# Kernel tuning notes

Hardware: AMD Instinct MI355X
Metric: run time of the kernel (lower is better)

## Reference

```python
import jax, jax.numpy as jnp
import numpy as np

B, C, H, W = 128, 512, 14, 14
P = 512  # num_parts (codebook size)


def setup_inputs() -> dict:
    key = jax.random.key(0)
    k1, k2, k3 = jax.random.split(key, 3)
    fm = jax.random.normal(k1, (B, C, H, W), dtype=jnp.float32)
    embedding = jax.random.normal(k2, (B, C), dtype=jnp.float32)
    # self.w = torch.randn(P, C).clamp_(min=0)
    w = jnp.maximum(jax.random.normal(k3, (P, C), dtype=jnp.float32), 0.0)
    w_ep_sum = w  # clone of w at init
    w_ep_num = jnp.ones((P,), dtype=jnp.float32)
    return {"fm": fm, "embedding": embedding, "w": w,
            "w_ep_sum": w_ep_sum, "w_ep_num": w_ep_num, "epoch": 5}


def reference(fm, embedding, w, w_ep_sum, w_ep_num, epoch):
    b, c, h, wd = fm.shape
    p = w.shape[0]
    # NCHW -> [B, HW, C]
    x = jnp.transpose(fm, (0, 2, 3, 1)).reshape(b, h * wd, c)
    xf = x.reshape(b * h * wd, c)
    dist = (jnp.sum(xf * xf, axis=1, keepdims=True)
            + jnp.sum(w * w, axis=1)
            - 2.0 * (xf @ w.T))                      # [B*HW, P]
    assign = jax.nn.softmax(-dist.reshape(b, h * wd, p), axis=-1)
    # hard threshold: zero out weak assignments
    assign = jnp.where(assign < 1.0 / p, 0.0, assign)  # [B, HW, P]
    assign_sum = assign.mean(axis=1)                    # [B, P]

    if epoch > 2:  # epoch is a static Python int
        # relu(einsum('bn,nc->bnc').mean(1)) == relu((assign_sum @ w) / P)
        cvec = jax.nn.relu((assign_sum @ w) / p)        # [B, C]
        embedding_cat = jnp.concatenate([embedding, cvec], axis=-1)
    else:
        embedding_cat = jnp.concatenate([embedding, jnp.zeros_like(embedding)], axis=-1)

    # collect_weight (no-grad EMA-style accumulate).
    # einsum('bmn,bmc->bmnc').sum(1).sum(0) == einsum('bmn,bmc->nc') -- avoids
    # materializing the [B,M,N,C] tensor the torch code builds.
    update_w = jnp.einsum('bmn,bmc->nc', assign, x)     # [P, C]
    assign_mean = jnp.sum(assign, axis=(0, 1))          # [P]
    upd = assign_mean > 1.0
    new_w_ep_sum = jnp.where(upd[:, None], w_ep_sum + update_w, w_ep_sum)
    new_w_ep_num = jnp.where(upd, w_ep_num + assign_mean, w_ep_num)
    return embedding_cat, new_w_ep_sum, new_w_ep_num
```

## Files before the change

### kernel.cpp

```cpp
#include <hip/hip_runtime.h>
#include <hip/hip_bf16.h>

#define Bn   128
#define Cn   512
#define HWn  196
#define Mn   25088
#define Pn   512
#define MPAD 32768
#define SPLITK2 32
#define KCH  1024

#define OFF_XT     0u
#define OFF_AT     8388608u
#define OFF_PART   16777216u
#define OFF_XMT    16777216u
#define OFF_WF     25165824u
#define OFF_WNORM  25296896u
#define OFF_RAWP   25297408u
#define OFF_MEAN   25559552u

#define OUT_CAT  0u
#define OUT_WSUM 131072u
#define OUT_WNUM 393216u

using bf16x8 = __attribute__((ext_vector_type(8))) short;
using f16x8  = __attribute__((ext_vector_type(8))) _Float16;
using f32x4  = __attribute__((ext_vector_type(4))) float;

__device__ __forceinline__ unsigned short f2b(float f) {
    union { float f; unsigned u; } x; x.f = f;
    unsigned r = x.u + 0x7fffu + ((x.u >> 16) & 1u);
    return (unsigned short)(r >> 16);
}

__global__ __launch_bounds__(64) void k_wnorm(const float* __restrict__ w,
                                              float* __restrict__ wn,
                                              _Float16* __restrict__ wf) {
    int n = blockIdx.x, l = threadIdx.x;
    const float* p = w + (size_t)n * Cn + l * 8;
    float4 a = *(const float4*)p;
    float4 b = *(const float4*)(p + 4);
    float s = a.x*a.x + a.y*a.y + a.z*a.z + a.w*a.w
            + b.x*b.x + b.y*b.y + b.z*b.z + b.w*b.w;
    alignas(16) _Float16 h[8];
    h[0]=(_Float16)a.x; h[1]=(_Float16)a.y; h[2]=(_Float16)a.z; h[3]=(_Float16)a.w;
    h[4]=(_Float16)b.x; h[5]=(_Float16)b.y; h[6]=(_Float16)b.z; h[7]=(_Float16)b.w;
    *(float4*)(wf + (size_t)(n >> 4) * 8192u + (size_t)(l >> 2) * 512
                 + (n & 15) * 32 + (l & 3) * 8) = *(const float4*)h;
    #pragma unroll
    for (int o = 32; o > 0; o >>= 1) s += __shfl_down(s, o);
    if (l == 0) wn[n] = s;
}

__global__ __launch_bounds__(512) void k_prep2(const float* __restrict__ fm,
                                               _Float16* __restrict__ xmt,
                                               unsigned short* __restrict__ xt) {
    __shared__ _Float16 tile[64][200];
    int b = blockIdx.x;
    int cg = blockIdx.y * 64;
    int t = threadIdx.x;
    for (int i = t; i < 64 * 49; i += 512) {
        int cl = i / 49, h4 = i - cl * 49;
        float4 v = *(const float4*)(fm + ((size_t)(b * Cn + cg + cl) * HWn) + h4 * 4);
        tile[cl][h4*4+0] = (_Float16)v.x;
        tile[cl][h4*4+1] = (_Float16)v.y;
        tile[cl][h4*4+2] = (_Float16)v.z;
        tile[cl][h4*4+3] = (_Float16)v.w;
    }
    __syncthreads();
    for (int i = t; i < 2048; i += 512) {
        int q = i >> 9, rem = i & 511, j = rem >> 3, cgi = rem & 7;
        alignas(16) _Float16 h[8];
        if (j < 49) {
            #pragma unroll
            for (int x = 0; x < 8; ++x) h[x] = tile[cgi * 8 + x][q * 49 + j];
        } else {
            #pragma unroll
            for (int x = 0; x < 8; ++x) h[x] = (_Float16)0.f;
        }
        int Ti = b * 16 + q * 4 + (j >> 4);
        int seg = (cg >> 5) + (cgi >> 2);
        int inner = (j & 15) * 32 + (cgi & 3) * 8;
        *(float4*)(xmt + (size_t)Ti * 8192u + (size_t)seg * 512 + inner) = *(const float4*)h;
    }
    for (int i = t; i < 64 * 4 * 16; i += 512) {
        int cl = i >> 6, rem = i & 63;
        int q = rem >> 4, j4 = rem & 15;
        ushort4 o;
        if (j4 < 12) {
            o.x = f2b((float)tile[cl][q*49 + j4*4 + 0]);
            o.y = f2b((float)tile[cl][q*49 + j4*4 + 1]);
            o.z = f2b((float)tile[cl][q*49 + j4*4 + 2]);
            o.w = f2b((float)tile[cl][q*49 + j4*4 + 3]);
        } else if (j4 == 12) {
            o.x = f2b((float)tile[cl][q*49 + 48]);
            o.y = 0; o.z = 0; o.w = 0;
        } else {
            o.x = 0; o.y = 0; o.z = 0; o.w = 0;
        }
        int c = cg + cl;
        int T = c >> 4;
        int seg = b * 8 + q * 2 + (j4 >> 3);
        int k = (j4 & 7) * 4;
        *(ushort4*)(xt + (size_t)T * 524288u + (size_t)seg * 512 + (c & 15) * 32 + k) = o;
    }
}

__global__ __launch_bounds__(512) void k_post(const _Float16* __restrict__ xmt,
                                              const _Float16* __restrict__ wf,
                                              const float* __restrict__ wnorm,
                                              unsigned short* __restrict__ at,
                                              float* __restrict__ rawp) {
    __shared__ float redmx[64][8];
    __shared__ float redsm[64][8];
    const int bid = blockIdx.x;
    const int b = bid >> 2, chunk = bid & 3;
    const int tid = threadIdx.x;
    const int nq = tid >> 6, lane = tid & 63;
    const int rl = lane & 15, rq = lane >> 4;
    const int loff = rl * 32 + rq * 8;
    const int n0 = nq * 64;

    const _Float16* pa[4];
    const _Float16* pb[4];
    #pragma unroll
    for (int f = 0; f < 4; ++f) {
        pa[f] = xmt + (size_t)(b * 16 + chunk * 4 + f) * 8192u + loff;
        pb[f] = wf  + (size_t)(nq * 4 + f) * 8192u + loff;
    }

    f32x4 acc[4][4] = {};
    f16x8 aC[4], bC[4], aN[4], bN[4];
    #pragma unroll
    for (int f = 0; f < 4; ++f) {
        aC[f] = *(const f16x8*)(pa[f]);
        bC[f] = *(const f16x8*)(pb[f]);
    }
    for (int seg = 0; seg < 16; seg += 2) {
        #pragma unroll
        for (int f = 0; f < 4; ++f) {
            aN[f] = *(const f16x8*)(pa[f] + (seg + 1) * 512);
            bN[f] = *(const f16x8*)(pb[f] + (seg + 1) * 512);
        }
        #pragma unroll
        for (int i = 0; i < 4; ++i)
            #pragma unroll
            for (int j = 0; j < 4; ++j)
                acc[i][j] = __builtin_amdgcn_mfma_f32_16x16x32_f16(aC[i], bC[j], acc[i][j], 0, 0, 0);
        if (seg + 2 < 16) {
            #pragma unroll
            for (int f = 0; f < 4; ++f) {
                aC[f] = *(const f16x8*)(pa[f] + (seg + 2) * 512);
                bC[f] = *(const f16x8*)(pb[f] + (seg + 2) * 512);
            }
        }
        #pragma unroll
        for (int i = 0; i < 4; ++i)
            #pragma unroll
            for (int j = 0; j < 4; ++j)
                acc[i][j] = __builtin_amdgcn_mfma_f32_16x16x32_f16(aN[i], bN[j], acc[i][j], 0, 0, 0);
    }
    float wn[4];
    #pragma unroll
    for (int g = 0; g < 4; ++g) wn[g] = wnorm[n0 + g * 16 + rl];
    #pragma unroll
    for (int f = 0; f < 4; ++f)
        #pragma unroll
        for (int g = 0; g < 4; ++g)
            #pragma unroll
            for (int r = 0; r < 4; ++r)
                acc[f][g][r] = 2.0f * acc[f][g][r] - wn[g];
    float mx[4][4];
    #pragma unroll
    for (int f = 0; f < 4; ++f)
        #pragma unroll
        for (int r = 0; r < 4; ++r) {
            float m_ = fmaxf(fmaxf(acc[f][0][r], acc[f][1][r]),
                             fmaxf(acc[f][2][r], acc[f][3][r]));
            #pragma unroll
            for (int o = 8; o >= 1; o >>= 1) m_ = fmaxf(m_, __shfl_xor(m_, o));
            mx[f][r] = m_;
        }
    if (rl == 0)
        #pragma unroll
        for (int f = 0; f < 4; ++f)
            #pragma unroll
            for (int r = 0; r < 4; ++r)
                redmx[f * 16 + rq * 4 + r][nq] = mx[f][r];
    __syncthreads();
    float rmax[4][4];
    #pragma unroll
    for (int f = 0; f < 4; ++f)
        #pragma unroll
        for (int r = 0; r < 4; ++r) {
            const float* q = redmx[f * 16 + rq * 4 + r];
            rmax[f][r] = fmaxf(fmaxf(fmaxf(q[0], q[1]), fmaxf(q[2], q[3])),
                               fmaxf(fmaxf(q[4], q[5]), fmaxf(q[6], q[7])));
        }
    float sm[4][4];
    #pragma unroll
    for (int f = 0; f < 4; ++f)
        #pragma unroll
        for (int r = 0; r < 4; ++r) {
            float s_ = 0.f;
            #pragma unroll
            for (int g = 0; g < 4; ++g) {
                float p = __expf(acc[f][g][r] - rmax[f][r]);
                acc[f][g][r] = p;
                s_ += p;
            }
            #pragma unroll
            for (int o = 8; o >= 1; o >>= 1) s_ += __shfl_xor(s_, o);
            sm[f][r] = s_;
        }
    if (rl == 0)
        #pragma unroll
        for (int f = 0; f < 4; ++f)
            #pragma unroll
            for (int r = 0; r < 4; ++r)
                redsm[f * 16 + rq * 4 + r][nq] = sm[f][r];
    __syncthreads();
    const float invP = 1.0f / 512.0f;
    #pragma unroll
    for (int f = 0; f < 4; ++f)
        #pragma unroll
        for (int r = 0; r < 4; ++r) {
            const float* q = redsm[f * 16 + rq * 4 + r];
            float inv = 1.0f / (q[0] + q[1] + q[2] + q[3] + q[4] + q[5] + q[6] + q[7]);
            #pragma unroll
            for (int g = 0; g < 4; ++g) {
                float a = acc[f][g][r] * inv;
                acc[f][g][r] = (a < invP) ? 0.0f : a;
            }
        }
    float cs[4] = {};
    #pragma unroll
    for (int g = 0; g < 4; ++g) {
        #pragma unroll
        for (int f = 0; f < 4; ++f)
            #pragma unroll
            for (int r = 0; r < 4; ++r)
                if (f * 16 + rq * 4 + r < 49) cs[g] += acc[f][g][r];
        cs[g] += __shfl_xor(cs[g], 16);
        cs[g] += __shfl_xor(cs[g], 32);
    }
    if (rq == 0)
        #pragma unroll
        for (int g = 0; g < 4; ++g)
            rawp[(size_t)bid * 512 + n0 + g * 16 + rl] = cs[g];
    const int segb = b * 8 + chunk * 2;
    #pragma unroll
    for (int f = 0; f < 4; ++f) {
        const int mloc = f * 16 + rq * 4;
        const int sa = segb + (mloc >> 5);
        const int k = mloc & 31;
        #pragma unroll
        for (int g = 0; g < 4; ++g) {
            ushort4 o;
            o.x = (mloc + 0 < 49) ? f2b(acc[f][g][0]) : (unsigned short)0;
            o.y = (mloc + 1 < 49) ? f2b(acc[f][g][1]) : (unsigned short)0;
            o.z = (mloc + 2 < 49) ? f2b(acc[f][g][2]) : (unsigned short)0;
            o.w = (mloc + 3 < 49) ? f2b(acc[f][g][3]) : (unsigned short)0;
            const int T = nq * 4 + g;
            *(ushort4*)(at + (size_t)T * 524288u + (size_t)sa * 512 + rl * 32 + k) = o;
        }
    }
}

__global__ __launch_bounds__(256) void k_reduce(const float* __restrict__ rawp,
                                                const float* __restrict__ wnum,
                                                float* __restrict__ mean,
                                                float* __restrict__ outnum) {
    int n = blockIdx.x * 256 + threadIdx.x;
    float s = 0.f;
    for (int r = 0; r < 512; ++r) s += rawp[(size_t)r * Pn + n];
    mean[n] = s;
    outnum[n] = wnum[n] + (s > 1.0f ? s : 0.0f);
}

__global__ __launch_bounds__(256) void k_cvec(const float* __restrict__ rawp,
                                              const float* __restrict__ w,
                                              const float* __restrict__ emb,
                                              const int* __restrict__ epoch,
                                              float* __restrict__ out) {
    __shared__ float srow[512];
    int b = blockIdx.x, t = threadIdx.x;
    float s0 = 0.f, s1 = 0.f;
    #pragma unroll
    for (int q = 0; q < 4; ++q) {
        s0 += rawp[(size_t)(4 * b + q) * Pn + t];
        s1 += rawp[(size_t)(4 * b + q) * Pn + t + 256];
    }
    srow[t] = s0;
    srow[t + 256] = s1;
    __syncthreads();
    float a0 = 0.f, a1 = 0.f;
    for (int p = 0; p < Pn; ++p) {
        float ap = srow[p];
        a0 = fmaf(ap, w[(size_t)p * Cn + t], a0);
        a1 = fmaf(ap, w[(size_t)p * Cn + t + 256], a1);
    }
    const float sc = 1.0f / (196.0f * 512.0f);
    int ep = epoch[0];
    float c0 = (ep > 2) ? fmaxf(a0, 0.f) * sc : 0.f;
    float c1 = (ep > 2) ? fmaxf(a1, 0.f) * sc : 0.f;
    out[(size_t)b * 1024 + t]             = emb[(size_t)b * Cn + t];
    out[(size_t)b * 1024 + t + 256]       = emb[(size_t)b * Cn + t + 256];
    out[(size_t)b * 1024 + 512 + t]       = c0;
    out[(size_t)b * 1024 + 512 + t + 256] = c1;
}

__global__ __launch_bounds__(256) void k_upw_mfma(const unsigned short* __restrict__ at,
                                                  const unsigned short* __restrict__ xt,
                                                  float* __restrict__ part) {
    const int id = blockIdx.x;
    const int sp = id & 31;
    const int m  = id >> 5;
    const int tid = threadIdx.x;
    const int wave = tid >> 6, lane = tid & 63;
    const int wn = wave >> 1, wc = wave & 1;
    const int n0 = (m & 3) * 128;
    const int c0 = (m >> 2) * 128;
    const int rl = lane & 15, rq = lane >> 4;
    const int loff = rl * 32 + rq * 8;
    const int segbase = sp * 32;

    const unsigned short* pa[4];
    const unsigned short* pb[4];
    #pragma unroll
    for (int f = 0; f < 4; ++f) {
        const int Ta = (n0 >> 4) + wn * 4 + f;
        const int Tb = (c0 >> 4) + wc * 4 + f;
        pa[f] = at + (size_t)Ta * 524288u + (size_t)segbase * 512 + loff;
        pb[f] = xt + (size_t)Tb * 524288u + (size_t)segbase * 512 + loff;
    }

    f32x4 acc[4][4] = {};
    bf16x8 aC[4], bC[4], aN[4], bN[4];
    #pragma unroll
    for (int f = 0; f < 4; ++f) {
        aC[f] = *(const bf16x8*)(pa[f]);
        bC[f] = *(const bf16x8*)(pb[f]);
    }
    for (int ks = 0; ks < 32; ks += 2) {
        #pragma unroll
        for (int f = 0; f < 4; ++f) {
            aN[f] = *(const bf16x8*)(pa[f] + (ks + 1) * 512);
            bN[f] = *(const bf16x8*)(pb[f] + (ks + 1) * 512);
        }
        #pragma unroll
        for (int i = 0; i < 4; ++i)
            #pragma unroll
            for (int j = 0; j < 4; ++j)
                acc[i][j] = __builtin_amdgcn_mfma_f32_16x16x32_bf16(aC[i], bC[j], acc[i][j], 0, 0, 0);
        if (ks + 2 < 32) {
            #pragma unroll
            for (int f = 0; f < 4; ++f) {
                aC[f] = *(const bf16x8*)(pa[f] + (ks + 2) * 512);
                bC[f] = *(const bf16x8*)(pb[f] + (ks + 2) * 512);
            }
        }
        #pragma unroll
        for (int i = 0; i < 4; ++i)
            #pragma unroll
            for (int j = 0; j < 4; ++j)
                acc[i][j] = __builtin_amdgcn_mfma_f32_16x16x32_bf16(aN[i], bN[j], acc[i][j], 0, 0, 0);
    }
    float* o = part + (size_t)sp * (Pn * Cn);
    const int rq4 = rq * 4;
    #pragma unroll
    for (int i = 0; i < 4; ++i) {
        #pragma unroll
        for (int j = 0; j < 4; ++j) {
            int n = n0 + wn * 64 + i * 16 + rq4;
            int c = c0 + wc * 64 + j * 16 + rl;
            #pragma unroll
            for (int r = 0; r < 4; ++r)
                o[(size_t)(n + r) * Cn + c] = acc[i][j][r];
        }
    }
}

__global__ __launch_bounds__(256) void k_wep(const float* __restrict__ part,
                                             const float* __restrict__ mean,
                                             const float* __restrict__ wsum,
                                             float* __restrict__ out1) {
    int n = blockIdx.x, t = threadIdx.x;
    bool upd = mean[n] > 1.0f;
    #pragma unroll
    for (int cc = 0; cc < 2; ++cc) {
        int c = t + cc * 256;
        float s = 0.f;
        #pragma unroll
        for (int k = 0; k < SPLITK2; ++k)
            s += part[(size_t)k * (Pn * Cn) + (size_t)n * Cn + c];
        size_t idx = (size_t)n * Cn + c;
        out1[idx] = wsum[idx] + (upd ? s : 0.f);
    }
}

extern "C" void kernel_launch(void* const* d_in, const int* in_sizes, int n_in,
                              void* d_out, int out_size, void* d_ws, size_t ws_size,
                              hipStream_t stream) {
    const float* fm    = (const float*)d_in[0];
    const float* emb   = (const float*)d_in[1];
    const float* w     = (const float*)d_in[2];
    const float* wsum  = (const float*)d_in[3];
    const float* wnum  = (const float*)d_in[4];
    const int*   epoch = (const int*)d_in[5];
    float* out = (float*)d_out;
    float* wsf = (float*)d_ws;

    unsigned short* xtb   = (unsigned short*)(wsf + OFF_XT);
    unsigned short* atb   = (unsigned short*)(wsf + OFF_AT);
    float*          partb = wsf + OFF_PART;
    _Float16*       xmtb  = (_Float16*)(wsf + OFF_XMT);
    _Float16*       wfb   = (_Float16*)(wsf + OFF_WF);
    float*          wnormb = wsf + OFF_WNORM;
    float*          rawpb  = wsf + OFF_RAWP;
    float*          meanb  = wsf + OFF_MEAN;

    k_wnorm<<<512, 64, 0, stream>>>(w, wnormb, wfb);
    k_prep2<<<dim3(Bn, 8), 512, 0, stream>>>(fm, xmtb, xtb);
    k_post<<<512, 512, 0, stream>>>(xmtb, wfb, wnormb, atb, rawpb);
    k_reduce<<<2, 256, 0, stream>>>(rawpb, wnum, meanb, out + OUT_WNUM);
    k_cvec<<<Bn, 256, 0, stream>>>(rawpb, w, emb, epoch, out + OUT_CAT);
    k_upw_mfma<<<512, 256, 0, stream>>>(atb, xtb, partb);
    k_wep<<<Pn, 256, 0, stream>>>(partb, meanb, wsum, out + OUT_WSUM);
}
```

Before: 183.5 us.

## Store x row-major and stage A tiles through shared memory in distance GEMM

The prep kernel now writes the fp16 activation matrix as plain row-major [B*HW, C] with no padding, replacing the pre-tiled MFMA fragment layout. The distance/softmax kernel loads each 49x64 A chunk into LDS once per block and shares it across the 8 waves, instead of every wave reading its own copy of the A fragments from global memory. It also sets launch_bounds with a minimum of 2 blocks per CU. The cost is extra __syncthreads per K chunk and no register double-buffering of the next A/B loads, which may leave MFMA stalled on memory.

New measurement: 170.9 us, median of 2. 1.07x faster.

```diff
diff --git a/kernel.cpp b/kernel.cpp
--- a/kernel.cpp
+++ b/kernel.cpp
@@ -6,14 +6,13 @@
 #define HWn  196
 #define Mn   25088
 #define Pn   512
-#define MPAD 32768
 #define SPLITK2 32
 #define KCH  1024
 
 #define OFF_XT     0u
 #define OFF_AT     8388608u
 #define OFF_PART   16777216u
-#define OFF_XMT    16777216u
+#define OFF_XM     16777216u
 #define OFF_WF     25165824u
 #define OFF_WNORM  25296896u
 #define OFF_RAWP   25297408u
@@ -53,7 +52,7 @@
 }
 
 __global__ __launch_bounds__(512) void k_prep2(const float* __restrict__ fm,
-                                               _Float16* __restrict__ xmt,
+                                               _Float16* __restrict__ xm,
                                                unsigned short* __restrict__ xt) {
     __shared__ _Float16 tile[64][200];
     int b = blockIdx.x;
@@ -68,20 +67,12 @@
         tile[cl][h4*4+3] = (_Float16)v.w;
     }
     __syncthreads();
-    for (int i = t; i < 2048; i += 512) {
-        int q = i >> 9, rem = i & 511, j = rem >> 3, cgi = rem & 7;
+    for (int i = t; i < HWn * 8; i += 512) {
+        int hw = i >> 3, seg = i & 7;
         alignas(16) _Float16 h[8];
-        if (j < 49) {
-            #pragma unroll
-            for (int x = 0; x < 8; ++x) h[x] = tile[cgi * 8 + x][q * 49 + j];
-        } else {
-            #pragma unroll
-            for (int x = 0; x < 8; ++x) h[x] = (_Float16)0.f;
-        }
-        int Ti = b * 16 + q * 4 + (j >> 4);
-        int seg = (cg >> 5) + (cgi >> 2);
-        int inner = (j & 15) * 32 + (cgi & 3) * 8;
-        *(float4*)(xmt + (size_t)Ti * 8192u + (size_t)seg * 512 + inner) = *(const float4*)h;
+        #pragma unroll
+        for (int j = 0; j < 8; ++j) h[j] = tile[seg * 8 + j][hw];
+        *(float4*)(xm + (size_t)(b * HWn + hw) * Cn + cg + seg * 8) = *(const float4*)h;
     }
     for (int i = t; i < 64 * 4 * 16; i += 512) {
         int cl = i >> 6, rem = i & 63;
@@ -106,70 +97,71 @@
     }
 }
 
-__global__ __launch_bounds__(512) void k_post(const _Float16* __restrict__ xmt,
-                                              const _Float16* __restrict__ wf,
-                                              const float* __restrict__ wnorm,
-                                              unsigned short* __restrict__ at,
-                                              float* __restrict__ rawp) {
+__global__ __launch_bounds__(512, 2) void k_post(const _Float16* __restrict__ xm,
+                                                 const _Float16* __restrict__ wf,
+                                                 const float* __restrict__ wnorm,
+                                                 unsigned short* __restrict__ at,
+                                                 float* __restrict__ rawp) {
+    __shared__ _Float16 As[64][72];
     __shared__ float redmx[64][8];
     __shared__ float redsm[64][8];
     const int bid = blockIdx.x;
-    const int b = bid >> 2, chunk = bid & 3;
+    const int b = bid >> 2, q = bid & 3;
     const int tid = threadIdx.x;
     const int nq = tid >> 6, lane = tid & 63;
     const int rl = lane & 15, rq = lane >> 4;
-    const int loff = rl * 32 + rq * 8;
+    const int kb = rq * 8;
+    const int m0 = b * 196 + q * 49;
     const int n0 = nq * 64;
-
-    const _Float16* pa[4];
-    const _Float16* pb[4];
-    #pragma unroll
-    for (int f = 0; f < 4; ++f) {
-        pa[f] = xmt + (size_t)(b * 16 + chunk * 4 + f) * 8192u + loff;
-        pb[f] = wf  + (size_t)(nq * 4 + f) * 8192u + loff;
-    }
+    const int srow = tid >> 3;
+    const int skc  = tid & 7;
+    const bool sOK = srow < 49;
+    const _Float16* asrc = xm + (size_t)(m0 + srow) * Cn + skc * 8;
+
+    if (!sOK) {
+        f16x8 z = {};
+        *(f16x8*)&As[srow][skc * 8] = z;
+    }
+    if (sOK) *(f16x8*)&As[srow][skc * 8] = *(const f16x8*)asrc;
+    __syncthreads();
+
+    const _Float16* wtb = wf + (size_t)(nq * 4) * 8192u + rl * 32 + kb;
 
     f32x4 acc[4][4] = {};
-    f16x8 aC[4], bC[4], aN[4], bN[4];
-    #pragma unroll
-    for (int f = 0; f < 4; ++f) {
-        aC[f] = *(const f16x8*)(pa[f]);
-        bC[f] = *(const f16x8*)(pb[f]);
-    }
-    for (int seg = 0; seg < 16; seg += 2) {
-        #pragma unroll
-        for (int f = 0; f < 4; ++f) {
-            aN[f] = *(const f16x8*)(pa[f] + (seg + 1) * 512);
-            bN[f] = *(const f16x8*)(pb[f] + (seg + 1) * 512);
-        }
-        #pragma unroll
-        for (int i = 0; i < 4; ++i)
-            #pragma unroll
-            for (int j = 0; j < 4; ++j)
-                acc[i][j] = __builtin_amdgcn_mfma_f32_16x16x32_f16(aC[i], bC[j], acc[i][j], 0, 0, 0);
-        if (seg + 2 < 16) {
-            #pragma unroll
-            for (int f = 0; f < 4; ++f) {
-                aC[f] = *(const f16x8*)(pa[f] + (seg + 2) * 512);
-                bC[f] = *(const f16x8*)(pb[f] + (seg + 2) * 512);
-            }
-        }
-        #pragma unroll
-        for (int i = 0; i < 4; ++i)
-            #pragma unroll
-            for (int j = 0; j < 4; ++j)
-                acc[i][j] = __builtin_amdgcn_mfma_f32_16x16x32_f16(aN[i], bN[j], acc[i][j], 0, 0, 0);
-    }
-    float wn[4];
-    #pragma unroll
-    for (int g = 0; g < 4; ++g) wn[g] = wnorm[n0 + g * 16 + rl];
+    for (int c = 0; c < 8; ++c) {
+        #pragma unroll
+        for (int ks = 0; ks < 2; ++ks) {
+            const int seg = c * 2 + ks;
+            f16x8 a[4], bb[4];
+            #pragma unroll
+            for (int f = 0; f < 4; ++f)
+                a[f] = *(const f16x8*)&As[f * 16 + rl][ks * 32 + kb];
+            #pragma unroll
+            for (int g = 0; g < 4; ++g)
+                bb[g] = *(const f16x8*)(wtb + (size_t)g * 8192u + seg * 512);
+            #pragma unroll
+            for (int f = 0; f < 4; ++f)
+                #pragma unroll
+                for (int g = 0; g < 4; ++g)
+                    acc[f][g] = __builtin_amdgcn_mfma_f32_16x16x32_f16(a[f], bb[g], acc[f][g], 0, 0, 0);
+        }
+        if (c < 7) {
+            __syncthreads();
+            if (sOK)
+                *(f16x8*)&As[srow][skc * 8] = *(const f16x8*)(asrc + (c + 1) * 64);
+            __syncthreads();
+        }
+    }
+    float wn4[4];
+    #pragma unroll
+    for (int g = 0; g < 4; ++g) wn4[g] = wnorm[n0 + g * 16 + rl];
     #pragma unroll
     for (int f = 0; f < 4; ++f)
         #pragma unroll
         for (int g = 0; g < 4; ++g)
             #pragma unroll
             for (int r = 0; r < 4; ++r)
-                acc[f][g][r] = 2.0f * acc[f][g][r] - wn[g];
+                acc[f][g][r] = 2.0f * acc[f][g][r] - wn4[g];
     float mx[4][4];
     #pragma unroll
     for (int f = 0; f < 4; ++f)
@@ -193,9 +185,9 @@
     for (int f = 0; f < 4; ++f)
         #pragma unroll
         for (int r = 0; r < 4; ++r) {
-            const float* q = redmx[f * 16 + rq * 4 + r];
-            rmax[f][r] = fmaxf(fmaxf(fmaxf(q[0], q[1]), fmaxf(q[2], q[3])),
-                               fmaxf(fmaxf(q[4], q[5]), fmaxf(q[6], q[7])));
+            const float* p = redmx[f * 16 + rq * 4 + r];
+            rmax[f][r] = fmaxf(fmaxf(fmaxf(p[0], p[1]), fmaxf(p[2], p[3])),
+                               fmaxf(fmaxf(p[4], p[5]), fmaxf(p[6], p[7])));
         }
     float sm[4][4];
     #pragma unroll
@@ -225,8 +217,8 @@
     for (int f = 0; f < 4; ++f)
         #pragma unroll
         for (int r = 0; r < 4; ++r) {
-            const float* q = redsm[f * 16 + rq * 4 + r];
-            float inv = 1.0f / (q[0] + q[1] + q[2] + q[3] + q[4] + q[5] + q[6] + q[7]);
+            const float* p = redsm[f * 16 + rq * 4 + r];
+            float inv = 1.0f / (p[0] + p[1] + p[2] + p[3] + p[4] + p[5] + p[6] + p[7]);
             #pragma unroll
             for (int g = 0; g < 4; ++g) {
                 float a = acc[f][g][r] * inv;
@@ -248,11 +240,11 @@
         #pragma unroll
         for (int g = 0; g < 4; ++g)
             rawp[(size_t)bid * 512 + n0 + g * 16 + rl] = cs[g];
-    const int segb = b * 8 + chunk * 2;
+    const int segbase = b * 8 + q * 2;
     #pragma unroll
     for (int f = 0; f < 4; ++f) {
         const int mloc = f * 16 + rq * 4;
-        const int sa = segb + (mloc >> 5);
+        const int sa = segbase + (mloc >> 5);
         const int k = mloc & 31;
         #pragma unroll
         for (int g = 0; g < 4; ++g) {
@@ -414,15 +406,15 @@
     unsigned short* xtb   = (unsigned short*)(wsf + OFF_XT);
     unsigned short* atb   = (unsigned short*)(wsf + OFF_AT);
     float*          partb = wsf + OFF_PART;
-    _Float16*       xmtb  = (_Float16*)(wsf + OFF_XMT);
+    _Float16*       xmb   = (_Float16*)(wsf + OFF_XM);
     _Float16*       wfb   = (_Float16*)(wsf + OFF_WF);
     float*          wnormb = wsf + OFF_WNORM;
     float*          rawpb  = wsf + OFF_RAWP;
     float*          meanb  = wsf + OFF_MEAN;
 
     k_wnorm<<<512, 64, 0, stream>>>(w, wnormb, wfb);
-    k_prep2<<<dim3(Bn, 8), 512, 0, stream>>>(fm, xmtb, xtb);
-    k_post<<<512, 512, 0, stream>>>(xmtb, wfb, wnormb, atb, rawpb);
+    k_prep2<<<dim3(Bn, 8), 512, 0, stream>>>(fm, xmb, xtb);
+    k_post<<<512, 512, 0, stream>>>(xmb, wfb, wnormb, atb, rawpb);
     k_reduce<<<2, 256, 0, stream>>>(rawpb, wnum, meanb, out + OUT_WNUM);
     k_cvec<<<Bn, 256, 0, stream>>>(rawpb, w, emb, epoch, out + OUT_CAT);
     k_upw_mfma<<<512, 256, 0, stream>>>(atb, xtb, partb);
```
